# Kernel tuning notes

Hardware: AMD Instinct MI355X
Metric: run time of the kernel (lower is better)

## Reference

```python
import jax, jax.numpy as jnp
import numpy as np

NEG = -100.0  # MaxPlusSemiring.zero
V, E = 50000, 300
B, L = 64, 512
P, M = 200, 7          # num patterns, pattern length
D = M * 2 * P          # diag rows
H, C = 100, 2          # mlp hidden, classes


def setup_inputs() -> dict:
    key = jax.random.key(0)
    ks = jax.random.split(key, 12)
    diags = jax.random.normal(ks[1], (D, E), jnp.float32)
    diags = diags / jnp.linalg.norm(diags, axis=1, keepdims=True)  # normalize() in __init__
    return {
        "docs": jax.random.randint(ks[0], (B, L), 0, V),
        "embeddings": jax.random.normal(ks[2], (V, E), jnp.float32),
        "diags": diags,
        "bias": jax.random.normal(ks[3], (D,), jnp.float32),
        "epsilon": jax.random.normal(ks[4], (P, M - 1), jnp.float32),
        "w1": jax.random.normal(ks[5], (P, H), jnp.float32) * 0.05,
        "b1": jnp.zeros((H,), jnp.float32),
        "w2": jax.random.normal(ks[6], (H, H), jnp.float32) * 0.05,
        "b2": jnp.zeros((H,), jnp.float32),
        "w3": jax.random.normal(ks[7], (H, C), jnp.float32) * 0.05,
        "b3": jnp.zeros((C,), jnp.float32),
    }


def _sopa(docs, embeddings, diags, bias, epsilon, w1, b1, w2, b2, w3, b3):
    # transition scores: semiring.from_float = identity for MaxPlus
    emb = embeddings[docs]                                   # [B,L,E]
    ts = jnp.einsum('ble,de->bld', emb, diags) + bias        # [B,L,D]
    T = ts.reshape(B, L, P, 2, M)                            # [B,L,P,diag,M]

    h0 = jnp.full((B, P, M), NEG, ts.dtype).at[:, :, 0].set(0.0)  # one at start state
    s0 = jnp.full((B, P), NEG, ts.dtype)
    zero_pad = jnp.full((B, P, 1), NEG, ts.dtype)            # semiring.zero
    restart = jnp.zeros((B, P, 1), ts.dtype)                 # semiring.one
    eps = epsilon[None]                                      # eps_scale=0 -> identity; [1,P,M-1]

    def step(carry, x):  # x: [B,P,2,M]
        h, s = carry
        after_eps = jnp.maximum(h, jnp.concatenate([zero_pad, h[:, :, :-1] + eps], axis=2))
        main = jnp.concatenate([restart, after_eps[:, :, :-1] + x[:, :, 1, :-1]], axis=2)
        self_loop = after_eps + x[:, :, 0, :]                # self_loop_scale = 0 (identity)
        h_new = jnp.maximum(main, self_loop)
        s_new = jnp.maximum(s, h_new[:, :, -1])              # end state = M-1 for all patterns
        return (h_new, s_new), None

    (_, scores), _ = jax.lax.scan(step, (h0, s0), jnp.moveaxis(T, 1, 0))

    hidden = jax.nn.relu(scores @ w1 + b1)
    hidden = jax.nn.relu(hidden @ w2 + b2)
    return jax.nn.log_softmax(hidden @ w3 + b3, axis=-1)


def reference(docs, embeddings, diags, bias, epsilon, w1, b1, w2, b2, w3, b3):
    return _sopa(docs, embeddings, diags, bias, epsilon, w1, b1, w2, b2, w3, b3)
```

## Files before the change

kernel.cpp:

```cpp
#include <hip/hip_runtime.h>
#include <stdint.h>

#define NEG (-100.0f)

#define NE 300
#define NB 64
#define NL 512
#define NP 200
#define ND 2800
#define NDP 2816
#define NH 100

#define KP 320
#define UNITS 40
#define ROWB 640

#define PT 8
#define DT 112
#define NTILE 25
#define LC 32
#define NCHUNK 16
#define SCW 36

#define LDS_A   (LC*ROWB)
#define LDS_SC  (DT*SCW*4)
#define LDS_TOTAL (3*LDS_A + 2*LDS_SC)

using f32x4  = __attribute__((ext_vector_type(4))) float;
using bf16x8 = __attribute__((ext_vector_type(8))) __bf16;

#define SBAR()       asm volatile("s_barrier" ::: "memory")
#define WAIT_LGKM0() do { asm volatile("s_waitcnt lgkmcnt(0)" ::: "memory"); \
                          __builtin_amdgcn_sched_barrier(0); } while (0)
#define WAIT_VM(N)   do { asm volatile("s_waitcnt vmcnt(" #N ")" ::: "memory"); \
                          __builtin_amdgcn_sched_barrier(0); } while (0)

static __device__ __forceinline__ void gload16(const void* g, void* l) {
    __builtin_amdgcn_global_load_lds(
        (const __attribute__((address_space(1))) void*)g,
        (__attribute__((address_space(3))) void*)l, 16, 0, 0);
}

static __device__ __forceinline__ uint16_t f2bf(float f) {
    union { float f; uint32_t u; } v; v.f = f;
    return (uint16_t)((v.u + 0x7FFFu + ((v.u >> 16) & 1u)) >> 16);
}

static __device__ __forceinline__ void pin(bf16x8& x) {
    asm volatile("" : "+v"(x));
}

static __device__ __forceinline__ float dpp_shr1(float x) {
    int r = __builtin_amdgcn_update_dpp(0, __float_as_int(x), 0x111, 0xF, 0xF, true);
    return __int_as_float(r);
}

__global__ void prep_kernel(const int* __restrict__ docs,
                            const float* __restrict__ emb,
                            const float* __restrict__ diags,
                            const float* __restrict__ bias,
                            uint16_t* __restrict__ A_ws,
                            uint16_t* __restrict__ B_ws)
{
    int tid = blockIdx.x * blockDim.x + threadIdx.x;
    const int totalA = NB * NL * UNITS;
    const int total  = totalA + ND * UNITS;
    if (tid >= total) return;
    const float* src; uint16_t* dst; float extra; int r, j;
    if (tid < totalA) {
        r = tid / UNITS; j = tid - r * UNITS;
        src = emb + (size_t)docs[r] * NE;
        dst = A_ws + (size_t)r * KP;
        extra = 1.0f;
    } else {
        int t2 = tid - totalA;
        r = t2 / UNITS; j = t2 - r * UNITS;
        src = diags + (size_t)r * NE;
        dst = B_ws + (size_t)r * KP;
        extra = bias[r];
    }
    int jp = j ^ (r & 7);
    union { uint16_t h[8]; uint4 v; } u;
    if (j < 37) {
        float4 f0 = *reinterpret_cast<const float4*>(src + j * 8);
        float4 f1 = *reinterpret_cast<const float4*>(src + j * 8 + 4);
        u.h[0] = f2bf(f0.x); u.h[1] = f2bf(f0.y);
        u.h[2] = f2bf(f0.z); u.h[3] = f2bf(f0.w);
        u.h[4] = f2bf(f1.x); u.h[5] = f2bf(f1.y);
        u.h[6] = f2bf(f1.z); u.h[7] = f2bf(f1.w);
    } else if (j == 37) {
        float4 f0 = *reinterpret_cast<const float4*>(src + 296);
        u.h[0] = f2bf(f0.x); u.h[1] = f2bf(f0.y);
        u.h[2] = f2bf(f0.z); u.h[3] = f2bf(f0.w);
        u.h[4] = f2bf(extra); u.h[5] = 0; u.h[6] = 0; u.h[7] = 0;
    } else {
        u.v = uint4{0, 0, 0, 0};
    }
    *reinterpret_cast<uint4*>(dst + (size_t)jp * 8) = u.v;
}

template<int NFR>
static __device__ __forceinline__ void mfma_body(const char* __restrict__ Ab,
    const bf16x8 (&breg)[40], float* __restrict__ scw,
    int abase, int aswz, int cb, int rlo, int kq, int wr)
{
    f32x4 acc[NFR];
#pragma unroll
    for (int f = 0; f < NFR; ++f) acc[f] = f32x4{0.f, 0.f, 0.f, 0.f};
#pragma unroll
    for (int kk = 0; kk < KP / 32; ++kk) {
        int ab = abase + kk * 64 + kq * 16;
        bf16x8 av = *reinterpret_cast<const bf16x8*>(Ab + (ab ^ aswz));
#pragma unroll
        for (int f = 0; f < NFR; ++f)
            acc[f] = __builtin_amdgcn_mfma_f32_16x16x32_bf16(av, breg[f * 10 + kk], acc[f], 0, 0, 0);
    }
    const int crow = wr * 16 + kq * 4;
#pragma unroll
    for (int f = 0; f < NFR; ++f) {
        int col = (cb + f) * 16 + rlo;
        *reinterpret_cast<f32x4*>(scw + col * SCW + crow) = acc[f];
    }
}

static __device__ __forceinline__ void scan_chunk(const float* __restrict__ sc,
        float& h, float& s, float eps_r, bool is_m0, int i0, int i1)
{
    f32x4 xav[8], xbv[8];
#pragma unroll
    for (int i = 0; i < 8; ++i)
        xav[i] = *reinterpret_cast<const f32x4*>(sc + i0 * SCW + i * 4);
#pragma unroll
    for (int i = 0; i < 8; ++i)
        xbv[i] = *reinterpret_cast<const f32x4*>(sc + i1 * SCW + i * 4);
#pragma unroll
    for (int l = 0; l < LC; ++l) {
        float xa = xav[l >> 2][l & 3];
        float xb = xbv[l >> 2][l & 3];
        float hm1  = dpp_shr1(h);
        float t    = is_m0 ? NEG : (hm1 + eps_r);
        float ae   = fmaxf(h, t);
        float aem1 = dpp_shr1(ae);
        float mn   = is_m0 ? 0.0f : (aem1 + xb);
        h = fmaxf(mn, ae + xa);
        s = fmaxf(s, h);
    }
}

__global__ __launch_bounds__(512, 2)
void sopa_kernel(const uint16_t* __restrict__ A_ws,
                 const uint16_t* __restrict__ B_ws,
                 const float* __restrict__ epsilon,
                 float* __restrict__ scores_g)
{
    extern __shared__ char smem[];

    const int blk = blockIdx.x;
    const int bb  = blk / NTILE;
    const int pt  = blk - bb * NTILE;
    const int d0  = pt * DT;
    const int p0  = pt * PT;

    const int tid  = threadIdx.x;
    const int wave = tid >> 6;
    const int lane = tid & 63;

    const int rlo = lane & 15;
    const int kq  = lane >> 4;
    const int wr  = wave & 1;
    const int wc  = (wave >> 1) & 1;
    const int cb  = wc * 4;
    const int arow  = wr * 16 + rlo;
    const int abase = arow * ROWB;
    const int aswz  = (arow & 7) << 4;

    bf16x8 breg[40];
    if (wave < 4) {
        const uint16_t* Bg = B_ws + (size_t)d0 * KP;
#pragma unroll
        for (int f = 0; f < 4; ++f) {
#pragma unroll
            for (int kk = 0; kk < 10; ++kk) {
                const int col = (cb + f) * 16 + rlo;
                const int jp  = (kk * 4 + kq) ^ (col & 7);
                breg[f * 10 + kk] = *reinterpret_cast<const bf16x8*>(
                    Bg + (size_t)col * KP + jp * 8);
                pin(breg[f * 10 + kk]);
            }
        }
    }

    const int  q  = lane >> 3;
    const int  mm = lane & 7;
    const int  pl = ((wave == 5) ? 4 : 0) + (q & 3);
    const bool is_m0 = (mm == 0);
    float eps_r = 0.0f;
    if (mm >= 1 && mm <= 6) eps_r = epsilon[(p0 + pl) * 6 + (mm - 1)];
    const int i0 = pl * 14 + mm;
    const int i1 = pl * 14 + 7 + (mm ? mm - 1 : 0);
    float h = is_m0 ? 0.0f : NEG;
    float s = NEG;

    const int   wv    = wave & 1;
    const char* a_src = (const char*)(A_ws + (size_t)bb * NL * KP) + wv * 10240 + lane * 16;

    if (wave >= 6) {
#pragma unroll
        for (int i = 0; i < 10; ++i)
            gload16(a_src + i * 1024, smem + wv * 10240 + i * 1024);
#pragma unroll
        for (int i = 0; i < 10; ++i)
            gload16(a_src + LC * ROWB + i * 1024, smem + LDS_A + wv * 10240 + i * 1024);
        WAIT_VM(10);
    }
    SBAR();

    for (int c = 0; c < NCHUNK; ++c) {
        if (wave < 4) {
            const char* Ab  = smem + (c % 3) * LDS_A;
            float*      scw = (float*)(smem + 3 * LDS_A + (c & 1) * LDS_SC);
            if (wc == 0) mfma_body<4>(Ab, breg, scw, abase, aswz, cb, rlo, kq, wr);
            else         mfma_body<3>(Ab, breg, scw, abase, aswz, cb, rlo, kq, wr);
            WAIT_LGKM0();
            SBAR();
        } else if (wave < 6) {
            if (c > 0) {
                const float* scr = (const float*)(smem + 3 * LDS_A + ((c - 1) & 1) * LDS_SC);
                scan_chunk(scr, h, s, eps_r, is_m0, i0, i1);
            }
            SBAR();
        } else {
            if (c + 2 < NCHUNK) {
                const char* src = a_src + (size_t)(c + 2) * LC * ROWB;
                char*       lb  = smem + ((c + 2) % 3) * LDS_A + wv * 10240;
#pragma unroll
                for (int i = 0; i < 10; ++i)
                    gload16(src + i * 1024, lb + i * 1024);
                WAIT_VM(10);
            } else {
                WAIT_VM(0);
            }
            SBAR();
        }
    }

    if (wave == 4 || wave == 5) {
        const float* scr = (const float*)(smem + 3 * LDS_A + ((NCHUNK - 1) & 1) * LDS_SC);
        scan_chunk(scr, h, s, eps_r, is_m0, i0, i1);
        if (q < 4 && mm == 6) scores_g[bb * NP + p0 + pl] = s;
    }
}

__global__ void mlp_kernel(const float* __restrict__ scores_g,
                           const float* __restrict__ w1, const float* __restrict__ b1,
                           const float* __restrict__ w2, const float* __restrict__ b2,
                           const float* __restrict__ w3, const float* __restrict__ b3,
                           float* __restrict__ out)
{
    __shared__ float sc[NP];
    __shared__ float h1[NH];
    __shared__ float h2[NH];
    int b = blockIdx.x, t = threadIdx.x;
    for (int i = t; i < NP; i += blockDim.x) sc[i] = scores_g[b * NP + i];
    __syncthreads();
    if (t < NH) {
        float acc = b1[t];
#pragma unroll 8
        for (int k = 0; k < NP; ++k) acc += sc[k] * w1[k * NH + t];
        h1[t] = fmaxf(acc, 0.0f);
    }
    __syncthreads();
    if (t < NH) {
        float acc = b2[t];
#pragma unroll 8
        for (int k = 0; k < NH; ++k) acc += h1[k] * w2[k * NH + t];
        h2[t] = fmaxf(acc, 0.0f);
    }
    __syncthreads();
    if (t < 64) {
        float l0 = 0.0f, l1 = 0.0f;
        for (int k = t; k < NH; k += 64) {
            float hv = h2[k];
            l0 += hv * w3[k * 2];
            l1 += hv * w3[k * 2 + 1];
        }
#pragma unroll
        for (int off = 32; off > 0; off >>= 1) {
            l0 += __shfl_down(l0, off);
            l1 += __shfl_down(l1, off);
        }
        if (t == 0) {
            l0 += b3[0]; l1 += b3[1];
            float mx  = fmaxf(l0, l1);
            float lse = mx + logf(expf(l0 - mx) + expf(l1 - mx));
            out[b * 2 + 0] = l0 - lse;
            out[b * 2 + 1] = l1 - lse;
        }
    }
}

extern "C" void kernel_launch(void* const* d_in, const int* in_sizes, int n_in,
                              void* d_out, int out_size, void* d_ws, size_t ws_size,
                              hipStream_t stream)
{
    const int*   docs  = (const int*)  d_in[0];
    const float* emb   = (const float*)d_in[1];
    const float* diags = (const float*)d_in[2];
    const float* bias  = (const float*)d_in[3];
    const float* eps   = (const float*)d_in[4];
    const float* w1 = (const float*)d_in[5];
    const float* b1 = (const float*)d_in[6];
    const float* w2 = (const float*)d_in[7];
    const float* b2 = (const float*)d_in[8];
    const float* w3 = (const float*)d_in[9];
    const float* b3 = (const float*)d_in[10];
    float* out = (float*)d_out;

    char* ws = (char*)d_ws;
    uint16_t* A_ws     = (uint16_t*)ws;
    uint16_t* B_ws     = (uint16_t*)(ws + 20971520);
    float*    scores_g = (float*)   (ws + 20971520 + 1802240);

    {
        int totalUnits = (NB * NL + ND) * UNITS;
        int blocks = (totalUnits + 255) / 256;
        prep_kernel<<<blocks, 256, 0, stream>>>(docs, emb, diags, bias, A_ws, B_ws);
    }

    (void)hipFuncSetAttribute(reinterpret_cast<const void*>(sopa_kernel),
                              hipFuncAttributeMaxDynamicSharedMemorySize, LDS_TOTAL);
    sopa_kernel<<<NB * NTILE, 512, LDS_TOTAL, stream>>>(A_ws, B_ws, eps, scores_g);

    mlp_kernel<<<NB, 128, 0, stream>>>(scores_g, w1, b1, w2, b2, w3, b3, out);
}
```

Baseline: 303.7 us.

## Switch GEMM waves to 32x32x16 MFMA with padded per-tile B rows

The four compute waves now each own 32 diag columns of a tile padded from 112 to 128 rows. They use 32x32x16 bf16 MFMA with 20 k-steps instead of a 2x2 wave grid of 16x16x32 fragments, and the prep kernel lays out B with zero padding per tile. Each wave's control flow is split into its own loop, separating the producer, MFMA and scan roles. This halves the B registers per wave and reduces A LDS reads per MFMA, but wave 3 computes mostly padded columns and does wasted MFMA work.

New measurement: 264.1 us. 13.0% less time.

```diff
diff --git a/kernel.cpp b/kernel.cpp
--- a/kernel.cpp
+++ b/kernel.cpp
@@ -7,8 +7,6 @@
 #define NB 64
 #define NL 512
 #define NP 200
-#define ND 2800
-#define NDP 2816
 #define NH 100
 
 #define KP 320
@@ -17,7 +15,9 @@
 
 #define PT 8
 #define DT 112
+#define DTP 128
 #define NTILE 25
+#define NBROWS (NTILE*DTP)
 #define LC 32
 #define NCHUNK 16
 #define SCW 36
@@ -27,6 +27,7 @@
 #define LDS_TOTAL (3*LDS_A + 2*LDS_SC)
 
 using f32x4  = __attribute__((ext_vector_type(4))) float;
+using f32x16 = __attribute__((ext_vector_type(16))) float;
 using bf16x8 = __attribute__((ext_vector_type(8))) __bf16;
 
 #define SBAR()       asm volatile("s_barrier" ::: "memory")
@@ -64,9 +65,10 @@
 {
     int tid = blockIdx.x * blockDim.x + threadIdx.x;
     const int totalA = NB * NL * UNITS;
-    const int total  = totalA + ND * UNITS;
+    const int total  = totalA + NBROWS * UNITS;
     if (tid >= total) return;
-    const float* src; uint16_t* dst; float extra; int r, j;
+    const float* src = nullptr; uint16_t* dst; float extra = 0.0f; int r, j;
+    bool valid = true;
     if (tid < totalA) {
         r = tid / UNITS; j = tid - r * UNITS;
         src = emb + (size_t)docs[r] * NE;
@@ -75,13 +77,21 @@
     } else {
         int t2 = tid - totalA;
         r = t2 / UNITS; j = t2 - r * UNITS;
-        src = diags + (size_t)r * NE;
         dst = B_ws + (size_t)r * KP;
-        extra = bias[r];
+        int lr = r & (DTP - 1);
+        if (lr < DT) {
+            int dr = (r >> 7) * DT + lr;
+            src = diags + (size_t)dr * NE;
+            extra = bias[dr];
+        } else {
+            valid = false;
+        }
     }
     int jp = j ^ (r & 7);
     union { uint16_t h[8]; uint4 v; } u;
-    if (j < 37) {
+    if (!valid) {
+        u.v = uint4{0, 0, 0, 0};
+    } else if (j < 37) {
         float4 f0 = *reinterpret_cast<const float4*>(src + j * 8);
         float4 f1 = *reinterpret_cast<const float4*>(src + j * 8 + 4);
         u.h[0] = f2bf(f0.x); u.h[1] = f2bf(f0.y);
@@ -99,30 +109,6 @@
     *reinterpret_cast<uint4*>(dst + (size_t)jp * 8) = u.v;
 }
 
-template<int NFR>
-static __device__ __forceinline__ void mfma_body(const char* __restrict__ Ab,
-    const bf16x8 (&breg)[40], float* __restrict__ scw,
-    int abase, int aswz, int cb, int rlo, int kq, int wr)
-{
-    f32x4 acc[NFR];
-#pragma unroll
-    for (int f = 0; f < NFR; ++f) acc[f] = f32x4{0.f, 0.f, 0.f, 0.f};
-#pragma unroll
-    for (int kk = 0; kk < KP / 32; ++kk) {
-        int ab = abase + kk * 64 + kq * 16;
-        bf16x8 av = *reinterpret_cast<const bf16x8*>(Ab + (ab ^ aswz));
-#pragma unroll
-        for (int f = 0; f < NFR; ++f)
-            acc[f] = __builtin_amdgcn_mfma_f32_16x16x32_bf16(av, breg[f * 10 + kk], acc[f], 0, 0, 0);
-    }
-    const int crow = wr * 16 + kq * 4;
-#pragma unroll
-    for (int f = 0; f < NFR; ++f) {
-        int col = (cb + f) * 16 + rlo;
-        *reinterpret_cast<f32x4*>(scw + col * SCW + crow) = acc[f];
-    }
-}
-
 static __device__ __forceinline__ void scan_chunk(const float* __restrict__ sc,
         float& h, float& s, float eps_r, bool is_m0, int i0, int i1)
 {
@@ -147,7 +133,7 @@
     }
 }
 
-__global__ __launch_bounds__(512, 2)
+__global__ __launch_bounds__(512) __attribute__((amdgpu_waves_per_eu(2, 2)))
 void sopa_kernel(const uint16_t* __restrict__ A_ws,
                  const uint16_t* __restrict__ B_ws,
                  const float* __restrict__ epsilon,
@@ -158,78 +144,91 @@
     const int blk = blockIdx.x;
     const int bb  = blk / NTILE;
     const int pt  = blk - bb * NTILE;
-    const int d0  = pt * DT;
     const int p0  = pt * PT;
 
     const int tid  = threadIdx.x;
     const int wave = tid >> 6;
     const int lane = tid & 63;
 
-    const int rlo = lane & 15;
-    const int kq  = lane >> 4;
-    const int wr  = wave & 1;
-    const int wc  = (wave >> 1) & 1;
-    const int cb  = wc * 4;
-    const int arow  = wr * 16 + rlo;
-    const int abase = arow * ROWB;
-    const int aswz  = (arow & 7) << 4;
-
-    bf16x8 breg[40];
     if (wave < 4) {
-        const uint16_t* Bg = B_ws + (size_t)d0 * KP;
-#pragma unroll
-        for (int f = 0; f < 4; ++f) {
-#pragma unroll
-            for (int kk = 0; kk < 10; ++kk) {
-                const int col = (cb + f) * 16 + rlo;
-                const int jp  = (kk * 4 + kq) ^ (col & 7);
-                breg[f * 10 + kk] = *reinterpret_cast<const bf16x8*>(
-                    Bg + (size_t)col * KP + jp * 8);
-                pin(breg[f * 10 + kk]);
-            }
-        }
-    }
-
-    const int  q  = lane >> 3;
-    const int  mm = lane & 7;
-    const int  pl = ((wave == 5) ? 4 : 0) + (q & 3);
-    const bool is_m0 = (mm == 0);
-    float eps_r = 0.0f;
-    if (mm >= 1 && mm <= 6) eps_r = epsilon[(p0 + pl) * 6 + (mm - 1)];
-    const int i0 = pl * 14 + mm;
-    const int i1 = pl * 14 + 7 + (mm ? mm - 1 : 0);
-    float h = is_m0 ? 0.0f : NEG;
-    float s = NEG;
-
-    const int   wv    = wave & 1;
-    const char* a_src = (const char*)(A_ws + (size_t)bb * NL * KP) + wv * 10240 + lane * 16;
-
-    if (wave >= 6) {
-#pragma unroll
-        for (int i = 0; i < 10; ++i)
-            gload16(a_src + i * 1024, smem + wv * 10240 + i * 1024);
-#pragma unroll
-        for (int i = 0; i < 10; ++i)
-            gload16(a_src + LC * ROWB + i * 1024, smem + LDS_A + wv * 10240 + i * 1024);
-        WAIT_VM(10);
-    }
-    SBAR();
-
-    for (int c = 0; c < NCHUNK; ++c) {
-        if (wave < 4) {
+        const int arow  = lane & 31;
+        const int khalf = lane >> 5;
+        const int col   = wave * 32 + arow;
+        const int abase = arow * ROWB;
+        const int ax3   = arow & 7;
+        const bool wr_ok = col < DT;
+
+        bf16x8 breg[20];
+        const uint16_t* Bg = B_ws + ((size_t)pt * DTP + col) * KP;
+#pragma unroll
+        for (int st = 0; st < 20; ++st) {
+            int jp = (st * 2 + khalf) ^ (col & 7);
+            breg[st] = *reinterpret_cast<const bf16x8*>(Bg + jp * 8);
+            pin(breg[st]);
+        }
+        SBAR();
+
+        for (int c = 0; c < NCHUNK; ++c) {
             const char* Ab  = smem + (c % 3) * LDS_A;
             float*      scw = (float*)(smem + 3 * LDS_A + (c & 1) * LDS_SC);
-            if (wc == 0) mfma_body<4>(Ab, breg, scw, abase, aswz, cb, rlo, kq, wr);
-            else         mfma_body<3>(Ab, breg, scw, abase, aswz, cb, rlo, kq, wr);
+            f32x16 acc;
+#pragma unroll
+            for (int i = 0; i < 16; ++i) acc[i] = 0.0f;
+#pragma unroll
+            for (int st = 0; st < 20; ++st) {
+                int jx = (st * 2 + khalf) ^ ax3;
+                bf16x8 av = *reinterpret_cast<const bf16x8*>(Ab + abase + jx * 16);
+                acc = __builtin_amdgcn_mfma_f32_32x32x16_bf16(av, breg[st], acc, 0, 0, 0);
+            }
+            if (wr_ok) {
+#pragma unroll
+                for (int g = 0; g < 4; ++g) {
+                    f32x4 v;
+                    v[0] = acc[g * 4 + 0]; v[1] = acc[g * 4 + 1];
+                    v[2] = acc[g * 4 + 2]; v[3] = acc[g * 4 + 3];
+                    *reinterpret_cast<f32x4*>(scw + col * SCW + g * 8 + khalf * 4) = v;
+                }
+            }
             WAIT_LGKM0();
             SBAR();
-        } else if (wave < 6) {
+        }
+    } else if (wave < 6) {
+        const int  q  = lane >> 3;
+        const int  mm = lane & 7;
+        const int  pl = ((wave == 5) ? 4 : 0) + (q & 3);
+        const bool is_m0 = (mm == 0);
+        float eps_r = 0.0f;
+        if (mm >= 1 && mm <= 6) eps_r = epsilon[(p0 + pl) * 6 + (mm - 1)];
+        const int i0 = pl * 14 + mm;
+        const int i1 = pl * 14 + 7 + (mm ? mm - 1 : 0);
+        float h = is_m0 ? 0.0f : NEG;
+        float s = NEG;
+
+        SBAR();
+        for (int c = 0; c < NCHUNK; ++c) {
             if (c > 0) {
                 const float* scr = (const float*)(smem + 3 * LDS_A + ((c - 1) & 1) * LDS_SC);
                 scan_chunk(scr, h, s, eps_r, is_m0, i0, i1);
             }
             SBAR();
-        } else {
+        }
+        const float* scr = (const float*)(smem + 3 * LDS_A + ((NCHUNK - 1) & 1) * LDS_SC);
+        scan_chunk(scr, h, s, eps_r, is_m0, i0, i1);
+        if (q < 4 && mm == 6) scores_g[bb * NP + p0 + pl] = s;
+    } else {
+        const int   wv    = wave & 1;
+        const char* a_src = (const char*)(A_ws + (size_t)bb * NL * KP) + wv * 10240 + lane * 16;
+
+#pragma unroll
+        for (int i = 0; i < 10; ++i)
+            gload16(a_src + i * 1024, smem + wv * 10240 + i * 1024);
+#pragma unroll
+        for (int i = 0; i < 10; ++i)
+            gload16(a_src + LC * ROWB + i * 1024, smem + LDS_A + wv * 10240 + i * 1024);
+        WAIT_VM(10);
+        SBAR();
+
+        for (int c = 0; c < NCHUNK; ++c) {
             if (c + 2 < NCHUNK) {
                 const char* src = a_src + (size_t)(c + 2) * LC * ROWB;
                 char*       lb  = smem + ((c + 2) % 3) * LDS_A + wv * 10240;
@@ -242,12 +241,6 @@
             }
             SBAR();
         }
-    }
-
-    if (wave == 4 || wave == 5) {
-        const float* scr = (const float*)(smem + 3 * LDS_A + ((NCHUNK - 1) & 1) * LDS_SC);
-        scan_chunk(scr, h, s, eps_r, is_m0, i0, i1);
-        if (q < 4 && mm == 6) scores_g[bb * NP + p0 + pl] = s;
     }
 }
 
@@ -319,10 +312,10 @@
     char* ws = (char*)d_ws;
     uint16_t* A_ws     = (uint16_t*)ws;
     uint16_t* B_ws     = (uint16_t*)(ws + 20971520);
-    float*    scores_g = (float*)   (ws + 20971520 + 1802240);
+    float*    scores_g = (float*)   (ws + 20971520 + 2048000);
 
     {
-        int totalUnits = (NB * NL + ND) * UNITS;
+        int totalUnits = (NB * NL + NBROWS) * UNITS;
         int blocks = (totalUnits + 255) / 256;
         prep_kernel<<<blocks, 256, 0, stream>>>(docs, emb, diags, bias, A_ws, B_ws);
     }
```
